# Performance work log

Hardware: AMD Instinct MI355X
Metric: run time of the kernel (lower is better)

Reference implementation:

```python
import jax, jax.numpy as jnp
import numpy as np
from jax import lax

B, ENC, H, E, V = 16, 64, 96, 128, 32000

def _same_pad(k):
    # PyTorch padding='same' (stride=1): low = (k-1)//2, high = (k-1) - low
    t = k - 1
    return (t // 2, t - t // 2)

def _conv(x, w, pad):
    return lax.conv_general_dilated(x, w, (1, 1), pad,
                                    dimension_numbers=('NCHW', 'OIHW', 'NCHW'))

def setup_inputs() -> dict:
    key = jax.random.key(0)
    ks = jax.random.split(key, 16)
    s = 0.05
    return {
        'encoder_outputs': jax.random.normal(ks[0], (B, ENC, H), jnp.float32),
        'input_ids': jax.random.randint(ks[1], (B,), 0, V),
        'hidden': jax.random.normal(ks[2], (1, B, H), jnp.float32),
        'coverage': jnp.zeros((B, ENC), jnp.float32),
        'emb': jax.random.normal(ks[3], (V, E), jnp.float32) * s,
        'W_dec': jax.random.normal(ks[4], (H, H), jnp.float32) * s,
        'b_dec': jnp.zeros((H,), jnp.float32),
        'attn_w': jax.random.normal(ks[5], (ENC, ENC, H, H), jnp.float32) * 0.003,
        'attn_b': jnp.zeros((ENC,), jnp.float32),
        'cvg_w': jax.random.normal(ks[6], (ENC, ENC, 1, H), jnp.float32) * s,
        'cvg_b': jnp.zeros((ENC,), jnp.float32),
        'v': jax.random.normal(ks[7], (B, H), jnp.float32) * s,
        'W_new': jax.random.normal(ks[8], (H, H + E), jnp.float32) * s,
        'b_new': jnp.zeros((H,), jnp.float32),
        'w_ih': jax.random.normal(ks[9], (3 * H, H), jnp.float32) * s,
        'w_hh': jax.random.normal(ks[10], (3 * H, H), jnp.float32) * s,
        'b_ih': jnp.zeros((3 * H,), jnp.float32),
        'b_hh': jnp.zeros((3 * H,), jnp.float32),
        'W_pre': jax.random.normal(ks[11], (H, 2 * H), jnp.float32) * s,
        'b_pre': jnp.zeros((H,), jnp.float32),
        'W_out': jax.random.normal(ks[12], (V, H), jnp.float32) * s,
        'b_out': jnp.zeros((V,), jnp.float32),
    }

def _attn(hidden, enc_out, coverage, W_dec, b_dec, attn_w, attn_b, cvg_w, cvg_b, v):
    # AttnCalc.forward
    ph, pw = _same_pad(H), _same_pad(H)
    enc_feat = _conv(enc_out.reshape(B, ENC, 1, H), attn_w, (ph, pw))
    enc_feat = enc_feat + attn_b[None, :, None, None]          # (B,ENC,1,H)
    dec_feat = (hidden[0] @ W_dec.T + b_dec).reshape(B, 1, 1, H)
    cvg_feat = _conv(coverage.reshape(B, ENC, 1, 1), cvg_w, ((0, 0), _same_pad(H)))
    cvg_feat = cvg_feat + cvg_b[None, :, None, None]           # (B,ENC,1,1)
    feats = jnp.tanh((enc_feat + dec_feat + cvg_feat).reshape(B, ENC, H))
    attn_weights = jax.nn.softmax(jnp.einsum('beh,bh->be', feats, v), axis=1)
    new_cov = coverage + attn_weights                          # in-place += in torch
    ctx = jnp.einsum('be,beh->bh', attn_weights, enc_out)      # (B,H)
    return ctx, attn_weights, new_cov

def reference(encoder_outputs, input_ids, hidden, coverage, emb, W_dec, b_dec,
              attn_w, attn_b, cvg_w, cvg_b, v, W_new, b_new,
              w_ih, w_hh, b_ih, b_hh, W_pre, b_pre, W_out, b_out):
    embedded = emb[input_ids]                                  # (B,E); dropout = identity (eval)
    ctx1, _, cov1 = _attn(hidden, encoder_outputs, coverage,
                          W_dec, b_dec, attn_w, attn_b, cvg_w, cvg_b, v)
    x = jnp.concatenate([embedded, ctx1], axis=1) @ W_new.T + b_new   # (B,H)
    # single GRU step (PyTorch gate order: r, z, n)
    h = hidden[0]
    gi = x @ w_ih.T + b_ih
    gh = h @ w_hh.T + b_hh
    r = jax.nn.sigmoid(gi[:, :H] + gh[:, :H])
    z = jax.nn.sigmoid(gi[:, H:2 * H] + gh[:, H:2 * H])
    n = jnp.tanh(gi[:, 2 * H:] + r * gh[:, 2 * H:])
    h_new = (1.0 - z) * n + z * h                              # (B,H)
    hidden_new = h_new[None]                                   # (1,B,H)
    ctx2, aw2, cov2 = _attn(hidden_new, encoder_outputs, cov1,
                            W_dec, b_dec, attn_w, attn_b, cvg_w, cvg_b, v)
    o = jnp.tanh(jnp.concatenate([h_new, ctx2], axis=1) @ W_pre.T + b_pre)
    logp = jax.nn.log_softmax(o @ W_out.T + b_out, axis=1)     # (B,V)
    return (logp, hidden_new, ctx2, aw2, cov2)
```

## Files before the change

kernel.cpp:

```cpp
#include <hip/hip_runtime.h>

#define BB 16
#define ENC 64
#define HH 96
#define EE 128
#define VV 32000

__device__ __forceinline__ float tanh_fast(float x) {
    float e = __expf(2.f * x);
    return 1.f - 2.f / (e + 1.f);
}
__device__ __forceinline__ float sigmoid_fast(float x) {
    return 1.f / (1.f + __expf(-x));
}

#define STEP(q, wa, wb_, wc_, wd_) do { \
    accA.x += q.x*wa.x  + q.y*wa.y  + q.z*wa.z  + q.w*wa.w;  \
    accA.y += q.x*wa.y  + q.y*wa.z  + q.z*wa.w  + q.w*wb_.x; \
    accA.z += q.x*wa.z  + q.y*wa.w  + q.z*wb_.x + q.w*wb_.y; \
    accA.w += q.x*wa.w  + q.y*wb_.x + q.z*wb_.y + q.w*wb_.z; \
    accB.x += q.x*wb_.x + q.y*wb_.y + q.z*wb_.z + q.w*wb_.w; \
    accB.y += q.x*wb_.y + q.y*wb_.z + q.z*wb_.w + q.w*wc_.x; \
    accB.z += q.x*wb_.z + q.y*wb_.w + q.z*wc_.x + q.w*wc_.y; \
    accB.w += q.x*wb_.w + q.y*wc_.x + q.z*wc_.y + q.w*wc_.z; \
    accC.x += q.x*wc_.x + q.y*wc_.y + q.z*wc_.z + q.w*wc_.w; \
    accC.y += q.x*wc_.y + q.y*wc_.z + q.z*wc_.w + q.w*wd_.x; \
    accC.z += q.x*wc_.z + q.y*wc_.w + q.z*wd_.x + q.w*wd_.y; \
    accC.w += q.x*wc_.w + q.y*wd_.x + q.z*wd_.y + q.w*wd_.z; \
} while (0)

__global__ __launch_bounds__(128) void k_encfeat(
    const float* __restrict__ enc,
    const float* __restrict__ attn_w,
    const float* __restrict__ cvg_w,
    float* __restrict__ part,
    float* __restrict__ cvgw47)
{
    int blk = blockIdx.x;
    int b   = blk >> 6;
    int ot  = (blk >> 4) & 3;
    int ic  = blk & 15;
    int o0  = ot * 16;
    int i0  = ic * 4;
    int t   = threadIdx.x;

    __shared__ __align__(16) float encS[4 * 208];
    __shared__ __align__(16) float Wb[4 * 16 * 100];

    for (int f = t; f < 208; f += 128)
        ((float4*)encS)[f] = make_float4(0.f, 0.f, 0.f, 0.f);
    __syncthreads();
    for (int f = t; f < 4 * 96; f += 128) {
        int i = f / 96, j = f - i * 96;
        encS[i * 208 + 47 + j] = enc[(size_t)((b * ENC + i0 + i) * 96) + j];
    }
    for (int F = t; F < 1536; F += 128) {
        int o = F / 96;
        int r = F - o * 96;
        int i = r / 24, kq = r - i * 24;
        float4 q = *(const float4*)(attn_w +
            (size_t)((o0 + o) * ENC + (i0 + i)) * (96 * 96) + 47 * 96 + 4 * kq);
        *(float4*)&Wb[(i * 16 + o) * 100 + 4 * kq] = q;
    }
    if (b == 0 && ot == 0 && ic < 8) {
        #pragma unroll
        for (int j = 0; j < 4; ++j) {
            int e = ic * 512 + j * 128 + t;
            cvgw47[e] = cvg_w[(size_t)e * 96 + 47];
        }
    }
    __syncthreads();

    int w    = t >> 6;
    int ln   = t & 63;
    int og   = ln & 7;
    int xs   = ln >> 3;
    int x0   = xs * 12;
    int orow = w * 8 + og;

    float4 accA = make_float4(0.f, 0.f, 0.f, 0.f);
    float4 accB = make_float4(0.f, 0.f, 0.f, 0.f);
    float4 accC = make_float4(0.f, 0.f, 0.f, 0.f);

    for (int i = 0; i < 4; ++i) {
        const float* er = &encS[i * 208 + x0];
        const float* wr = &Wb[(i * 16 + orow) * 100];
        float4 e0 = *(const float4*)(er);
        float4 e1 = *(const float4*)(er + 4);
        float4 e2 = *(const float4*)(er + 8);
        float4 e3 = *(const float4*)(er + 12);
        #pragma unroll
        for (int cb = 0; cb < 6; ++cb) {
            float4 q0 = *(const float4*)(wr + 16 * cb);
            float4 q1 = *(const float4*)(wr + 16 * cb + 4);
            float4 q2 = *(const float4*)(wr + 16 * cb + 8);
            float4 q3 = *(const float4*)(wr + 16 * cb + 12);
            STEP(q0, e0, e1, e2, e3);
            e0 = *(const float4*)(er + 16 * cb + 16);
            STEP(q1, e1, e2, e3, e0);
            e1 = *(const float4*)(er + 16 * cb + 20);
            STEP(q2, e2, e3, e0, e1);
            e2 = *(const float4*)(er + 16 * cb + 24);
            STEP(q3, e3, e0, e1, e2);
            e3 = *(const float4*)(er + 16 * cb + 28);
        }
    }
    float* outr = part + ((size_t)(ic * 16 + b) * 64 + o0 + orow) * 96 + x0;
    *(float4*)(outr)     = accA;
    *(float4*)(outr + 4) = accB;
    *(float4*)(outr + 8) = accC;
}

__device__ __forceinline__ void matvec4(int g, int q, int nout, int nk,
    const float* __restrict__ W, int ldw, const float* __restrict__ bias,
    const float* __restrict__ xv, float* __restrict__ y)
{
    for (int j = g; j < nout; j += 64) {
        const float* wr = W + (size_t)j * ldw;
        float s = 0.f;
        for (int m = q; m < nk / 4; m += 4) {
            float4 wq = *(const float4*)(wr + 4 * m);
            s += wq.x * xv[4 * m] + wq.y * xv[4 * m + 1]
               + wq.z * xv[4 * m + 2] + wq.w * xv[4 * m + 3];
        }
        s += __shfl_xor(s, 1);
        s += __shfl_xor(s, 2);
        if (q == 0) y[j] = s + bias[j];
    }
}

__global__ __launch_bounds__(256) void k_fused(
    const float* __restrict__ enc, const int* __restrict__ ids,
    const float* __restrict__ hidden, const float* __restrict__ coverage,
    const float* __restrict__ emb,
    const float* __restrict__ W_dec, const float* __restrict__ b_dec,
    const float* __restrict__ attn_b,
    const float* __restrict__ cvgw47, const float* __restrict__ cvg_b,
    const float* __restrict__ vvec,
    const float* __restrict__ W_new, const float* __restrict__ b_new,
    const float* __restrict__ w_ih, const float* __restrict__ w_hh,
    const float* __restrict__ b_ih, const float* __restrict__ b_hh,
    const float* __restrict__ W_pre, const float* __restrict__ b_pre,
    const float* __restrict__ part, float* __restrict__ oG,
    float* __restrict__ out_hidden, float* __restrict__ out_ctx2,
    float* __restrict__ out_aw2, float* __restrict__ out_cov2)
{
    int b = blockIdx.x, t = threadIdx.x;
    int g = t >> 2, q = t & 3;

    __shared__ __align__(16) float efS[ENC * HH];
    __shared__ __align__(16) float encS[ENC * HH];
    __shared__ float hS[HH], vS[HH], decS[HH], ctxS[HH], xS[HH], h2S[HH], ctx2S[HH];
    __shared__ float covS[ENC], cvgS[ENC], sS[ENC], awS[ENC];
    __shared__ float embS[EE];
    __shared__ __align__(16) float xcatS[EE + HH];
    __shared__ float giS[3 * HH], ghS[3 * HH];

    {
        const float4* enc4 = (const float4*)(enc + (size_t)b * ENC * HH);
        float4* efS4  = (float4*)efS;
        float4* encS4 = (float4*)encS;
        for (int f = t; f < (ENC * HH) / 4; f += 256) {
            float4 s = make_float4(0.f, 0.f, 0.f, 0.f);
            #pragma unroll
            for (int ic = 0; ic < 16; ++ic) {
                const float4 p = *(const float4*)(part +
                    (size_t)(ic * 16 + b) * (ENC * HH) + 4 * f);
                s.x += p.x; s.y += p.y; s.z += p.z; s.w += p.w;
            }
            efS4[f]  = s;
            encS4[f] = enc4[f];
        }
    }
    if (t < HH) { hS[t] = hidden[b * HH + t]; vS[t] = vvec[b * HH + t]; }
    if (t >= 96 && t < 160) covS[t - 96] = coverage[b * ENC + (t - 96)];
    if (t >= 128 && t < 256) embS[t - 128] = emb[(size_t)ids[b] * EE + (t - 128)];
    __syncthreads();

    matvec4(g, q, HH, HH, W_dec, HH, b_dec, hS, decS);
    matvec4(g, q, ENC, ENC, cvgw47, ENC, cvg_b, covS, cvgS);
    __syncthreads();
    {
        int e = g;
        float base = attn_b[e] + cvgS[e];
        const float* efr = &efS[e * HH];
        float s = 0.f;
        for (int m = q; m < 24; m += 4) {
            #pragma unroll
            for (int u = 0; u < 4; ++u) {
                int xx = 4 * m + u;
                s += tanh_fast(efr[xx] + decS[xx] + base) * vS[xx];
            }
        }
        s += __shfl_xor(s, 1); s += __shfl_xor(s, 2);
        if (q == 0) sS[e] = s;
    }
    __syncthreads();
    if (t < ENC) {
        float m = -1e30f;
        for (int j = 0; j < ENC; ++j) m = fmaxf(m, sS[j]);
        float sum = 0.f;
        for (int j = 0; j < ENC; ++j) sum += __expf(sS[j] - m);
        float aw = __expf(sS[t] - m) / sum;
        awS[t] = aw;
        covS[t] += aw;
    }
    __syncthreads();
    if (t < HH) {
        float c = 0.f;
        for (int o = 0; o < ENC; ++o) c += awS[o] * encS[o * HH + t];
        ctxS[t] = c;
        xcatS[EE + t] = c;
    }
    if (t >= 128 && t < 256) xcatS[t - 128] = embS[t - 128];
    __syncthreads();

    matvec4(g, q, HH, EE + HH, W_new, EE + HH, b_new, xcatS, xS);
    __syncthreads();

    matvec4(g, q, 3 * HH, HH, w_ih, HH, b_ih, xS, giS);
    matvec4(g, q, 3 * HH, HH, w_hh, HH, b_hh, hS, ghS);
    __syncthreads();
    if (t < HH) {
        float r = sigmoid_fast(giS[t] + ghS[t]);
        float z = sigmoid_fast(giS[HH + t] + ghS[HH + t]);
        float n = tanh_fast(giS[2 * HH + t] + r * ghS[2 * HH + t]);
        float hn = (1.f - z) * n + z * hS[t];
        h2S[t] = hn;
        out_hidden[b * HH + t] = hn;
    }
    __syncthreads();

    matvec4(g, q, HH, HH, W_dec, HH, b_dec, h2S, decS);
    matvec4(g, q, ENC, ENC, cvgw47, ENC, cvg_b, covS, cvgS);
    __syncthreads();
    {
        int e = g;
        float base = attn_b[e] + cvgS[e];
        const float* efr = &efS[e * HH];
        float s = 0.f;
        for (int m = q; m < 24; m += 4) {
            #pragma unroll
            for (int u = 0; u < 4; ++u) {
                int xx = 4 * m + u;
                s += tanh_fast(efr[xx] + decS[xx] + base) * vS[xx];
            }
        }
        s += __shfl_xor(s, 1); s += __shfl_xor(s, 2);
        if (q == 0) sS[e] = s;
    }
    __syncthreads();
    if (t < ENC) {
        float m = -1e30f;
        for (int j = 0; j < ENC; ++j) m = fmaxf(m, sS[j]);
        float sum = 0.f;
        for (int j = 0; j < ENC; ++j) sum += __expf(sS[j] - m);
        float aw = __expf(sS[t] - m) / sum;
        awS[t] = aw;
        covS[t] += aw;
        out_aw2[b * ENC + t]  = aw;
        out_cov2[b * ENC + t] = covS[t];
    }
    __syncthreads();
    if (t < HH) {
        float c = 0.f;
        for (int o = 0; o < ENC; ++o) c += awS[o] * encS[o * HH + t];
        ctx2S[t] = c;
        out_ctx2[b * HH + t] = c;
        xcatS[t] = h2S[t];
        xcatS[HH + t] = c;
    }
    __syncthreads();

    for (int j = g; j < HH; j += 64) {
        const float* wr = W_pre + (size_t)j * (2 * HH);
        float s = 0.f;
        for (int m = q; m < (2 * HH) / 4; m += 4) {
            float4 wq = *(const float4*)(wr + 4 * m);
            s += wq.x * xcatS[4 * m] + wq.y * xcatS[4 * m + 1]
               + wq.z * xcatS[4 * m + 2] + wq.w * xcatS[4 * m + 3];
        }
        s += __shfl_xor(s, 1); s += __shfl_xor(s, 2);
        if (q == 0) oG[b * HH + j] = tanh_fast(s + b_pre[j]);
    }
}

__global__ __launch_bounds__(128) void k_logits(
    const float* __restrict__ oG, const float* __restrict__ W_out,
    const float* __restrict__ b_out, float* __restrict__ logits)
{
    __shared__ __align__(16) float oS[BB * HH];
    for (int i = threadIdx.x; i < BB * HH; i += 128) oS[i] = oG[i];
    __syncthreads();

    int v = blockIdx.x * 128 + threadIdx.x;
    const float4* row = (const float4*)(W_out + (size_t)v * HH);
    float acc[BB];
    #pragma unroll
    for (int b = 0; b < BB; ++b) acc[b] = 0.f;

    #pragma unroll 6
    for (int c = 0; c < HH / 4; ++c) {
        float4 qv = row[c];
        #pragma unroll
        for (int b = 0; b < BB; ++b) {
            const float4 o0 = *(const float4*)&oS[b * HH + c * 4];
            acc[b] += qv.x * o0.x + qv.y * o0.y + qv.z * o0.z + qv.w * o0.w;
        }
    }
    float bo = b_out[v];
    #pragma unroll
    for (int b = 0; b < BB; ++b) logits[b * VV + v] = acc[b] + bo;
}

#define MAX4(r) fmaxf(fmaxf((r).x, (r).y), fmaxf((r).z, (r).w))
__global__ __launch_bounds__(1024) void k_logsoftmax(float* __restrict__ out)
{
    int b = blockIdx.x, t = threadIdx.x;
    float* row = out + (size_t)b * VV;
    const float4* row4 = (const float4*)row;
    float4* row4w = (float4*)row;
    __shared__ float red[1024];

    float4 c0, c1, c2, c3, c4, c5, c6, c7;
    bool has7 = (t < 8000 - 7 * 1024);
    c0 = row4[t];
    c1 = row4[t + 1024];
    c2 = row4[t + 2048];
    c3 = row4[t + 3072];
    c4 = row4[t + 4096];
    c5 = row4[t + 5120];
    c6 = row4[t + 6144];
    float m0 = fmaxf(fmaxf(MAX4(c0), MAX4(c1)),
                     fmaxf(fmaxf(MAX4(c2), MAX4(c3)),
                           fmaxf(MAX4(c4), fmaxf(MAX4(c5), MAX4(c6)))));
    if (has7) { c7 = row4[t + 7168]; m0 = fmaxf(m0, MAX4(c7)); }
    red[t] = m0;
    __syncthreads();
    for (int s = 512; s > 0; s >>= 1) {
        if (t < s) red[t] = fmaxf(red[t], red[t + s]);
        __syncthreads();
    }
    float m = red[0]; __syncthreads();

    float s0 = 0.f;
    #define ESUM(r) (__expf((r).x - m) + __expf((r).y - m) + \
                     __expf((r).z - m) + __expf((r).w - m))
    s0 = ESUM(c0) + ESUM(c1) + ESUM(c2) + ESUM(c3)
       + ESUM(c4) + ESUM(c5) + ESUM(c6);
    if (has7) s0 += ESUM(c7);
    red[t] = s0;
    __syncthreads();
    for (int s = 512; s > 0; s >>= 1) {
        if (t < s) red[t] += red[t + s];
        __syncthreads();
    }
    float logZ = m + logf(red[0]);

    #define SUB4(r) { (r).x -= logZ; (r).y -= logZ; (r).z -= logZ; (r).w -= logZ; }
    SUB4(c0); SUB4(c1); SUB4(c2); SUB4(c3); SUB4(c4); SUB4(c5); SUB4(c6);
    row4w[t]        = c0;
    row4w[t + 1024] = c1;
    row4w[t + 2048] = c2;
    row4w[t + 3072] = c3;
    row4w[t + 4096] = c4;
    row4w[t + 5120] = c5;
    row4w[t + 6144] = c6;
    if (has7) { SUB4(c7); row4w[t + 7168] = c7; }
}

extern "C" void kernel_launch(void* const* d_in, const int* in_sizes, int n_in,
                              void* d_out, int out_size, void* d_ws, size_t ws_size,
                              hipStream_t stream) {
    const float* enc    = (const float*)d_in[0];
    const int*   ids    = (const int*)d_in[1];
    const float* hidden = (const float*)d_in[2];
    const float* cover  = (const float*)d_in[3];
    const float* emb    = (const float*)d_in[4];
    const float* W_dec  = (const float*)d_in[5];
    const float* b_dec  = (const float*)d_in[6];
    const float* attn_w = (const float*)d_in[7];
    const float* attn_b = (const float*)d_in[8];
    const float* cvg_w  = (const float*)d_in[9];
    const float* cvg_b  = (const float*)d_in[10];
    const float* vvec   = (const float*)d_in[11];
    const float* W_new  = (const float*)d_in[12];
    const float* b_new  = (const float*)d_in[13];
    const float* w_ih   = (const float*)d_in[14];
    const float* w_hh   = (const float*)d_in[15];
    const float* b_ih   = (const float*)d_in[16];
    const float* b_hh   = (const float*)d_in[17];
    const float* W_pre  = (const float*)d_in[18];
    const float* b_pre  = (const float*)d_in[19];
    const float* W_out  = (const float*)d_in[20];
    const float* b_out  = (const float*)d_in[21];

    float* wsf    = (float*)d_ws;
    float* oG     = wsf;
    float* cvgw47 = wsf + 1536;
    float* part   = wsf + 5632;

    float* out        = (float*)d_out;
    float* out_logp   = out;
    float* out_hidden = out + 512000;
    float* out_ctx2   = out + 513536;
    float* out_aw2    = out + 515072;
    float* out_cov2   = out + 516096;

    k_encfeat<<<1024, 128, 0, stream>>>(enc, attn_w, cvg_w, part, cvgw47);
    k_fused<<<16, 256, 0, stream>>>(enc, ids, hidden, cover, emb, W_dec, b_dec,
                                    attn_b, cvgw47, cvg_b, vvec, W_new, b_new,
                                    w_ih, w_hh, b_ih, b_hh, W_pre, b_pre,
                                    part, oG,
                                    out_hidden, out_ctx2, out_aw2, out_cov2);
    k_logits<<<250, 128, 0, stream>>>(oG, W_out, b_out, out_logp);
    k_logsoftmax<<<16, 1024, 0, stream>>>(out_logp);
}
```

Before: 345.2 us.

## Store encoder partials as bf16 and fuse softmax stats into logits kernel

The split-K partial sums of the encoder feature conv are now written as packed bf16 instead of fp32, halving the workspace traffic between k_encfeat and k_fused. The logits kernel also computes per-block row max and exp-sum, so the final log-softmax kernel only merges 250 partials per row and subtracts logZ across 256 blocks instead of 16. This replaces a full re-read and reduction of the logits by 16 large blocks with a more parallel pass. The cost is bf16 rounding in the attention features, which may hurt accuracy.

```diff
diff --git a/kernel.cpp b/kernel.cpp
--- a/kernel.cpp
+++ b/kernel.cpp
@@ -13,6 +13,15 @@
 __device__ __forceinline__ float sigmoid_fast(float x) {
     return 1.f / (1.f + __expf(-x));
 }
+__device__ __forceinline__ unsigned bf16pack(float a, float b) {
+    unsigned ua = __float_as_uint(a);
+    ua += 0x7FFFu + ((ua >> 16) & 1u);
+    unsigned ub = __float_as_uint(b);
+    ub += 0x7FFFu + ((ub >> 16) & 1u);
+    return (ua >> 16) | (ub & 0xFFFF0000u);
+}
+#define BF_LO(u) __uint_as_float((u) << 16)
+#define BF_HI(u) __uint_as_float((u) & 0xFFFF0000u)
 
 #define STEP(q, wa, wb_, wc_, wd_) do { \
     accA.x += q.x*wa.x  + q.y*wa.y  + q.z*wa.z  + q.w*wa.w;  \
@@ -33,7 +42,7 @@
     const float* __restrict__ enc,
     const float* __restrict__ attn_w,
     const float* __restrict__ cvg_w,
-    float* __restrict__ part,
+    unsigned short* __restrict__ part,
     float* __restrict__ cvgw47)
 {
     int blk = blockIdx.x;
@@ -105,10 +114,11 @@
             e3 = *(const float4*)(er + 16 * cb + 28);
         }
     }
-    float* outr = part + ((size_t)(ic * 16 + b) * 64 + o0 + orow) * 96 + x0;
-    *(float4*)(outr)     = accA;
-    *(float4*)(outr + 4) = accB;
-    *(float4*)(outr + 8) = accC;
+    unsigned* outp = (unsigned*)part +
+        ((size_t)(ic * 16 + b) * 6144 + (size_t)(o0 + orow) * 96 + x0) / 2;
+    *(uint2*)(outp)     = make_uint2(bf16pack(accA.x, accA.y), bf16pack(accA.z, accA.w));
+    *(uint2*)(outp + 2) = make_uint2(bf16pack(accB.x, accB.y), bf16pack(accB.z, accB.w));
+    *(uint2*)(outp + 4) = make_uint2(bf16pack(accC.x, accC.y), bf16pack(accC.z, accC.w));
 }
 
 __device__ __forceinline__ void matvec4(int g, int q, int nout, int nk,
@@ -141,7 +151,7 @@
     const float* __restrict__ w_ih, const float* __restrict__ w_hh,
     const float* __restrict__ b_ih, const float* __restrict__ b_hh,
     const float* __restrict__ W_pre, const float* __restrict__ b_pre,
-    const float* __restrict__ part, float* __restrict__ oG,
+    const unsigned short* __restrict__ part, float* __restrict__ oG,
     float* __restrict__ out_hidden, float* __restrict__ out_ctx2,
     float* __restrict__ out_aw2, float* __restrict__ out_cov2)
 {
@@ -157,20 +167,24 @@
     __shared__ float giS[3 * HH], ghS[3 * HH];
 
     {
-        const float4* enc4 = (const float4*)(enc + (size_t)b * ENC * HH);
-        float4* efS4  = (float4*)efS;
-        float4* encS4 = (float4*)encS;
-        for (int f = t; f < (ENC * HH) / 4; f += 256) {
-            float4 s = make_float4(0.f, 0.f, 0.f, 0.f);
+        const uint4* part4 = (const uint4*)part;
+        for (int f = t; f < 768; f += 256) {
+            float s0=0.f,s1=0.f,s2=0.f,s3=0.f,s4=0.f,s5=0.f,s6=0.f,s7=0.f;
             #pragma unroll
             for (int ic = 0; ic < 16; ++ic) {
-                const float4 p = *(const float4*)(part +
-                    (size_t)(ic * 16 + b) * (ENC * HH) + 4 * f);
-                s.x += p.x; s.y += p.y; s.z += p.z; s.w += p.w;
+                uint4 p = part4[(size_t)(ic * 16 + b) * 768 + f];
+                s0 += BF_LO(p.x); s1 += BF_HI(p.x);
+                s2 += BF_LO(p.y); s3 += BF_HI(p.y);
+                s4 += BF_LO(p.z); s5 += BF_HI(p.z);
+                s6 += BF_LO(p.w); s7 += BF_HI(p.w);
             }
-            efS4[f]  = s;
-            encS4[f] = enc4[f];
-        }
+            float4* d = (float4*)&efS[8 * f];
+            d[0] = make_float4(s0, s1, s2, s3);
+            d[1] = make_float4(s4, s5, s6, s7);
+        }
+        const float4* enc4 = (const float4*)(enc + (size_t)b * ENC * HH);
+        float4* encS4 = (float4*)encS;
+        for (int f = t; f < (ENC * HH) / 4; f += 256) encS4[f] = enc4[f];
     }
     if (t < HH) { hS[t] = hidden[b * HH + t]; vS[t] = vvec[b * HH + t]; }
     if (t >= 96 && t < 160) covS[t - 96] = coverage[b * ENC + (t - 96)];
@@ -287,13 +301,15 @@
 
 __global__ __launch_bounds__(128) void k_logits(
     const float* __restrict__ oG, const float* __restrict__ W_out,
-    const float* __restrict__ b_out, float* __restrict__ logits)
+    const float* __restrict__ b_out, float* __restrict__ logits,
+    float* __restrict__ pmax, float* __restrict__ psum)
 {
     __shared__ __align__(16) float oS[BB * HH];
     for (int i = threadIdx.x; i < BB * HH; i += 128) oS[i] = oG[i];
     __syncthreads();
 
-    int v = blockIdx.x * 128 + threadIdx.x;
+    int t = threadIdx.x;
+    int v = blockIdx.x * 128 + t;
     const float4* row = (const float4*)(W_out + (size_t)v * HH);
     float acc[BB];
     #pragma unroll
@@ -310,63 +326,77 @@
     }
     float bo = b_out[v];
     #pragma unroll
-    for (int b = 0; b < BB; ++b) logits[b * VV + v] = acc[b] + bo;
-}
-
-#define MAX4(r) fmaxf(fmaxf((r).x, (r).y), fmaxf((r).z, (r).w))
-__global__ __launch_bounds__(1024) void k_logsoftmax(float* __restrict__ out)
+    for (int b = 0; b < BB; ++b) {
+        acc[b] += bo;
+        logits[b * VV + v] = acc[b];
+    }
+
+    __shared__ float smx[2][BB], sms[2][BB];
+    int wv = t >> 6, ln = t & 63;
+    #pragma unroll
+    for (int b = 0; b < BB; ++b) {
+        float m = acc[b];
+        m = fmaxf(m, __shfl_xor(m, 1));
+        m = fmaxf(m, __shfl_xor(m, 2));
+        m = fmaxf(m, __shfl_xor(m, 4));
+        m = fmaxf(m, __shfl_xor(m, 8));
+        m = fmaxf(m, __shfl_xor(m, 16));
+        m = fmaxf(m, __shfl_xor(m, 32));
+        if (ln == 0) smx[wv][b] = m;
+    }
+    __syncthreads();
+    #pragma unroll
+    for (int b = 0; b < BB; ++b) {
+        float Mb = fmaxf(smx[0][b], smx[1][b]);
+        float s = __expf(acc[b] - Mb);
+        s += __shfl_xor(s, 1);
+        s += __shfl_xor(s, 2);
+        s += __shfl_xor(s, 4);
+        s += __shfl_xor(s, 8);
+        s += __shfl_xor(s, 16);
+        s += __shfl_xor(s, 32);
+        if (ln == 0) sms[wv][b] = s;
+    }
+    __syncthreads();
+    if (t < BB) {
+        pmax[blockIdx.x * BB + t] = fmaxf(smx[0][t], smx[1][t]);
+        psum[blockIdx.x * BB + t] = sms[0][t] + sms[1][t];
+    }
+}
+
+__global__ __launch_bounds__(256) void k_lsm(
+    float* __restrict__ logits,
+    const float* __restrict__ pmax, const float* __restrict__ psum)
 {
-    int b = blockIdx.x, t = threadIdx.x;
-    float* row = out + (size_t)b * VV;
-    const float4* row4 = (const float4*)row;
-    float4* row4w = (float4*)row;
-    __shared__ float red[1024];
-
-    float4 c0, c1, c2, c3, c4, c5, c6, c7;
-    bool has7 = (t < 8000 - 7 * 1024);
-    c0 = row4[t];
-    c1 = row4[t + 1024];
-    c2 = row4[t + 2048];
-    c3 = row4[t + 3072];
-    c4 = row4[t + 4096];
-    c5 = row4[t + 5120];
-    c6 = row4[t + 6144];
-    float m0 = fmaxf(fmaxf(MAX4(c0), MAX4(c1)),
-                     fmaxf(fmaxf(MAX4(c2), MAX4(c3)),
-                           fmaxf(MAX4(c4), fmaxf(MAX4(c5), MAX4(c6)))));
-    if (has7) { c7 = row4[t + 7168]; m0 = fmaxf(m0, MAX4(c7)); }
-    red[t] = m0;
-    __syncthreads();
-    for (int s = 512; s > 0; s >>= 1) {
-        if (t < s) red[t] = fmaxf(red[t], red[t + s]);
+    int blk = blockIdx.x;
+    int b = blk >> 4, s = blk & 15;
+    int t = threadIdx.x;
+    __shared__ float red[256];
+
+    float mt = (t < 250) ? pmax[t * BB + b] : -1e30f;
+    red[t] = mt;
+    __syncthreads();
+    for (int o = 128; o > 0; o >>= 1) {
+        if (t < o) red[t] = fmaxf(red[t], red[t + o]);
         __syncthreads();
     }
-    float m = red[0]; __syncthreads();
-
-    float s0 = 0.f;
-    #define ESUM(r) (__expf((r).x - m) + __expf((r).y - m) + \
-                     __expf((r).z - m) + __expf((r).w - m))
-    s0 = ESUM(c0) + ESUM(c1) + ESUM(c2) + ESUM(c3)
-       + ESUM(c4) + ESUM(c5) + ESUM(c6);
-    if (has7) s0 += ESUM(c7);
-    red[t] = s0;
-    __syncthreads();
-    for (int s = 512; s > 0; s >>= 1) {
-        if (t < s) red[t] += red[t + s];
+    float M = red[0];
+    __syncthreads();
+    float st = (t < 250) ? psum[t * BB + b] * __expf(mt - M) : 0.f;
+    red[t] = st;
+    __syncthreads();
+    for (int o = 128; o > 0; o >>= 1) {
+        if (t < o) red[t] += red[t + o];
         __syncthreads();
     }
-    float logZ = m + logf(red[0]);
-
-    #define SUB4(r) { (r).x -= logZ; (r).y -= logZ; (r).z -= logZ; (r).w -= logZ; }
-    SUB4(c0); SUB4(c1); SUB4(c2); SUB4(c3); SUB4(c4); SUB4(c5); SUB4(c6);
-    row4w[t]        = c0;
-    row4w[t + 1024] = c1;
-    row4w[t + 2048] = c2;
-    row4w[t + 3072] = c3;
-    row4w[t + 4096] = c4;
-    row4w[t + 5120] = c5;
-    row4w[t + 6144] = c6;
-    if (has7) { SUB4(c7); row4w[t + 7168] = c7; }
+    float logZ = M + logf(red[0]);
+
+    float4* row4 = (float4*)(logits + (size_t)b * VV);
+    for (int k = s * 500 + t; k < (s + 1) * 500; k += 256) {
+        float4 c = row4[k];
+        c.x -= logZ; c.y -= logZ; c.z -= logZ; c.w -= logZ;
+        row4[k] = c;
+    }
 }
 
 extern "C" void kernel_launch(void* const* d_in, const int* in_sizes, int n_in,
@@ -398,7 +428,9 @@
     float* wsf    = (float*)d_ws;
     float* oG     = wsf;
     float* cvgw47 = wsf + 1536;
-    float* part   = wsf + 5632;
+    float* pmax   = wsf + 5632;
+    float* psum   = wsf + 9632;
+    unsigned short* part = (unsigned short*)(wsf + 13632);
 
     float* out        = (float*)d_out;
     float* out_logp   = out;
@@ -413,6 +445,6 @@
                                     w_ih, w_hh, b_ih, b_hh, W_pre, b_pre,
                                     part, oG,
                                     out_hidden, out_ctx2, out_aw2, out_cov2);
-    k_logits<<<250, 128, 0, stream>>>(oG, W_out, b_out, out_logp);
-    k_logsoftmax<<<16, 1024, 0, stream>>>(out_logp);
-}
+    k_logits<<<250, 128, 0, stream>>>(oG, W_out, b_out, out_logp, pmax, psum);
+    k_lsm<<<256, 256, 0, stream>>>(out_logp, pmax, psum);
+}
```

New measurement: 349.1 us. No clear change (+1.1%).
